# Performance work log

Measured on AMD Instinct MI355X. Metric: run time of the kernel, lower is better.

## Reference

```python
import jax, jax.numpy as jnp
import numpy as np

N = 50000
E = 800000
NODE_CONT = 64
EDGE_CAT = 16
HID = 96
LAT = 64
NUM_LAYERS = 2
BN_EPS = 1e-5


def setup_inputs() -> dict:
    key = jax.random.key(0)
    ks = jax.random.split(key, 24)
    s = 0.05
    inp = {
        "x_cont": jax.random.normal(ks[0], (N, NODE_CONT), jnp.float32),
        "x_cat": jax.random.randint(ks[1], (N,), 0, 1),
        "edge_index": jax.random.randint(ks[2], (2, E), 0, N),
        "edge_attr_cat": jax.random.randint(ks[3], (E,), 0, EDGE_CAT),
        "edge_attr_cont": jax.random.normal(ks[4], (E, 1), jnp.float32),
        # parameters
        "w_node": jax.random.normal(ks[5], (HID, NODE_CONT), jnp.float32) * s,
        "b_node": jnp.zeros((HID,), jnp.float32),
        "edge_embed": jax.random.normal(ks[6], (EDGE_CAT, HID), jnp.float32) * s,
        "gcn_w": jax.random.normal(ks[7], (NUM_LAYERS, HID, HID), jnp.float32) * s,
        "gcn_b": jnp.zeros((NUM_LAYERS, HID), jnp.float32),
        "bn_gamma": jnp.ones((NUM_LAYERS, HID), jnp.float32),
        "bn_beta": jnp.zeros((NUM_LAYERS, HID), jnp.float32),
        "mlp_w1": jax.random.normal(ks[8], (NUM_LAYERS, HID, 2 * HID), jnp.float32) * s,
        "mlp_b1": jnp.zeros((NUM_LAYERS, HID), jnp.float32),
        "mlp_w2": jax.random.normal(ks[9], (NUM_LAYERS, HID, HID), jnp.float32) * s,
        "mlp_b2": jnp.zeros((NUM_LAYERS, HID), jnp.float32),
        "mu_w": jax.random.normal(ks[10], (LAT, HID), jnp.float32) * s,
        "mu_b": jnp.zeros((LAT,), jnp.float32),
        "lv_w": jax.random.normal(ks[11], (LAT, HID), jnp.float32) * s,
        "lv_b": jnp.zeros((LAT,), jnp.float32),
    }
    return inp


def _forward(x_cont, edge_index, edge_attr_cat,
             w_node, b_node, edge_embed,
             gcn_w, gcn_b, bn_gamma, bn_beta,
             mlp_w1, mlp_b1, mlp_w2, mlp_b2,
             mu_w, mu_b, lv_w, lv_b):
    n = x_cont.shape[0]
    # node embed (only continuous path active)
    h = x_cont @ w_node.T + b_node                      # [N, H]
    # edge embed (only categorical path active) -- memory-bound gather
    edge_h = edge_embed[edge_attr_cat]                  # [E, H]
    src, dst = edge_index[0], edge_index[1]
    # GCNConv: add self-loops, symmetric normalization
    loop = jnp.arange(n)
    src_f = jnp.concatenate([src, loop])
    dst_f = jnp.concatenate([dst, loop])
    deg = jax.ops.segment_sum(jnp.ones_like(dst_f, jnp.float32), dst_f, num_segments=n)
    dinv = jax.lax.rsqrt(deg)                           # deg >= 1 (self loops)
    norm = (dinv[src_f] * dinv[dst_f])[:, None]         # [E+N, 1]
    # edge_pooled: O(E) segment-mean replacing the O(N*E) python loop;
    # edge_h is constant across layers so compute it once.
    cnt = jax.ops.segment_sum(jnp.ones((edge_h.shape[0],), edge_h.dtype), dst, num_segments=n)
    pooled = jax.ops.segment_sum(edge_h, dst, num_segments=n) / jnp.maximum(cnt, 1.0)[:, None]
    for l in range(gcn_w.shape[0]):
        msg = (h @ gcn_w[l].T)[src_f] * norm            # gather + scale
        h_gnn = jax.ops.segment_sum(msg, dst_f, num_segments=n) + gcn_b[l]
        hc = jnp.concatenate([h_gnn, pooled], axis=-1)  # [N, 2H]
        h = jax.nn.relu(hc @ mlp_w1[l].T + mlp_b1[l]) @ mlp_w2[l].T + mlp_b2[l]
        # BatchNorm1d (training-mode batch stats, biased variance)
        mean = jnp.mean(h, axis=0)
        var = jnp.mean((h - mean) ** 2, axis=0)
        h = (h - mean) * jax.lax.rsqrt(var + BN_EPS) * bn_gamma[l] + bn_beta[l]
        h = jax.nn.relu(h)
        # dropout: eval mode (identity)
    mu = h @ mu_w.T + mu_b
    logvar = h @ lv_w.T + lv_b
    return mu, logvar


def reference(x_cont, x_cat, edge_index, edge_attr_cat, edge_attr_cont,
              w_node, b_node, edge_embed, gcn_w, gcn_b, bn_gamma, bn_beta,
              mlp_w1, mlp_b1, mlp_w2, mlp_b2, mu_w, mu_b, lv_w, lv_b):
    # x_cat and edge_attr_cont are unused: in_node_cat_dim=0, in_edge_cont_dim=0
    return _forward(x_cont, edge_index, edge_attr_cat,
                    w_node, b_node, edge_embed,
                    gcn_w, gcn_b, bn_gamma, bn_beta,
                    mlp_w1, mlp_b1, mlp_w2, mlp_b2,
                    mu_w, mu_b, lv_w, lv_b)
```

## Files before the change

kernel.cpp:

```cpp
#include <hip/hip_runtime.h>

#define N_NODES 50000
#define N_EDGES 800000
#define HID 96
#define NODE_CONT 64
#define LATD 64
#define EDGE_CATN 16
#define BN_EPS 1e-5f
#define CPAD 16
#define BCAP 48
#define MLP_BLOCKS 625
#define PPITCH 640

typedef __attribute__((ext_vector_type(8))) short bf16x8;
typedef __attribute__((ext_vector_type(4))) float f32x4;

__device__ __forceinline__ unsigned short f2bf(float f) {
    union { float f; unsigned u; } c; c.f = f;
    unsigned r = (c.u + 0x7fffu + ((c.u >> 16) & 1u)) >> 16;
    return (unsigned short)r;
}
__device__ __forceinline__ float bf2f(unsigned short u) {
    union { unsigned u; float f; } c; c.u = ((unsigned)u) << 16;
    return c.f;
}

__global__ void k_build(const int* __restrict__ ei, const int* __restrict__ ecat,
                        int* __restrict__ cnt, int* __restrict__ csr) {
    int e = blockIdx.x * blockDim.x + threadIdx.x;
    if (e >= N_EDGES) return;
    int dst = ei[N_EDGES + e];
    int r = atomicAdd(&cnt[dst * CPAD], 1);
    if (r < BCAP) csr[(size_t)dst * BCAP + r] = (ei[e] << 4) | (ecat[e] & 15);
}

template<int POOL>
__global__ __launch_bounds__(256) void k_aggregate(
    const int* __restrict__ csr, const int* __restrict__ cnt,
    const unsigned short* __restrict__ bt,
    const float* __restrict__ gcn_b, unsigned short* __restrict__ bgp,
    const float* __restrict__ eemb)
{
    __shared__ float s_eemb[EDGE_CATN * HID];
    if constexpr (POOL) {
        for (int i = threadIdx.x; i < EDGE_CATN * HID; i += 256)
            s_eemb[i] = eemb[i];
        __syncthreads();
    }
    int node = blockIdx.x * 8 + (threadIdx.x >> 5);
    int lane = threadIdx.x & 31;
    if (node >= N_NODES) return;
    int degr = cnt[node * CPAD];
    float dd = rsqrtf((float)(degr + 1));
    int deg = degr > BCAP ? BCAP : degr;
    const unsigned short* tn = bt + (size_t)node * HID;
    float a0 = bf2f(tn[lane]);
    float a1 = bf2f(tn[lane + 32]);
    float a2 = bf2f(tn[lane + 64]);
    float p0 = 0.f, p1 = 0.f, p2 = 0.f;
    int beg = node * BCAP, end = beg + deg;
    int p = beg;
    for (; p + 4 <= end; p += 4) {
        int e0 = csr[p], e1 = csr[p + 1], e2 = csr[p + 2], e3 = csr[p + 3];
        const unsigned short* r0 = bt + (size_t)(e0 >> 4) * HID;
        const unsigned short* r1 = bt + (size_t)(e1 >> 4) * HID;
        const unsigned short* r2 = bt + (size_t)(e2 >> 4) * HID;
        const unsigned short* r3 = bt + (size_t)(e3 >> 4) * HID;
        unsigned short v00 = r0[lane], v01 = r0[lane + 32], v02 = r0[lane + 64];
        unsigned short v10 = r1[lane], v11 = r1[lane + 32], v12 = r1[lane + 64];
        unsigned short v20 = r2[lane], v21 = r2[lane + 32], v22 = r2[lane + 64];
        unsigned short v30 = r3[lane], v31 = r3[lane + 32], v32 = r3[lane + 64];
        a0 += (bf2f(v00) + bf2f(v10)) + (bf2f(v20) + bf2f(v30));
        a1 += (bf2f(v01) + bf2f(v11)) + (bf2f(v21) + bf2f(v31));
        a2 += (bf2f(v02) + bf2f(v12)) + (bf2f(v22) + bf2f(v32));
        if constexpr (POOL) {
            const float* q0 = s_eemb + (e0 & 15) * HID;
            const float* q1 = s_eemb + (e1 & 15) * HID;
            const float* q2 = s_eemb + (e2 & 15) * HID;
            const float* q3 = s_eemb + (e3 & 15) * HID;
            p0 += (q0[lane] + q1[lane]) + (q2[lane] + q3[lane]);
            p1 += (q0[lane + 32] + q1[lane + 32]) + (q2[lane + 32] + q3[lane + 32]);
            p2 += (q0[lane + 64] + q1[lane + 64]) + (q2[lane + 64] + q3[lane + 64]);
        }
    }
    for (; p < end; ++p) {
        int e0 = csr[p];
        const unsigned short* r = bt + (size_t)(e0 >> 4) * HID;
        a0 += bf2f(r[lane]);
        a1 += bf2f(r[lane + 32]);
        a2 += bf2f(r[lane + 64]);
        if constexpr (POOL) {
            const float* q = s_eemb + (e0 & 15) * HID;
            p0 += q[lane]; p1 += q[lane + 32]; p2 += q[lane + 64];
        }
    }
    unsigned short* o = bgp + (size_t)node * 192;
    o[lane]      = f2bf(a0 * dd + gcn_b[lane]);
    o[lane + 32] = f2bf(a1 * dd + gcn_b[lane + 32]);
    o[lane + 64] = f2bf(a2 * dd + gcn_b[lane + 64]);
    if constexpr (POOL) {
        float inv = 1.f / (float)(deg < 1 ? 1 : deg);
        unsigned short* ob = o + 96;
        ob[lane]      = f2bf(p0 * inv);
        ob[lane + 32] = f2bf(p1 * inv);
        ob[lane + 64] = f2bf(p2 * inv);
    }
}

#define OFF_WNODE 0
#define OFF_GCN   6144
#define OFF_W1    24576
#define OFF_W2    61440
#define OFF_MU    79872
#define W_TOTAL   92160

__device__ __forceinline__ void wf_decode(int e, int K, int njt, int& j, int& k) {
    int t = e & 7;
    int lane = (e >> 3) & 63;
    int g = e >> 9;
    int kb = g / njt;
    int jt = g - kb * njt;
    j = jt * 16 + (lane & 15);
    k = kb * 32 + (lane >> 4) * 8 + t;
}

__global__ void k_wprep(const float* __restrict__ w_node, const float* __restrict__ gcn_w,
                        const float* __restrict__ w1, const float* __restrict__ w2,
                        const float* __restrict__ mu_w, const float* __restrict__ lv_w,
                        const float* __restrict__ b_node,
                        unsigned short* __restrict__ out, float* __restrict__ fused_b) {
    int i = blockIdx.x * blockDim.x + threadIdx.x;
    if (i < OFF_GCN) {
        int j, k;
        wf_decode(i, NODE_CONT, 6, j, k);
        float s = 0.f;
#pragma unroll 8
        for (int q = 0; q < HID; ++q) s += gcn_w[j * HID + q] * w_node[q * NODE_CONT + k];
        out[i] = f2bf(s);
    } else if (i < OFF_W1) {
        int e = i - OFF_GCN;
        int l = e / 9216; e -= l * 9216;
        int j, k;
        wf_decode(e, HID, 6, j, k);
        out[i] = f2bf(gcn_w[l * HID * HID + j * HID + k]);
    } else if (i < OFF_W2) {
        int e = i - OFF_W1;
        int l = e / 18432; e -= l * 18432;
        int j, k;
        wf_decode(e, 192, 6, j, k);
        out[i] = f2bf(w1[l * HID * 192 + j * 192 + k]);
    } else if (i < OFF_MU) {
        int e = i - OFF_W2;
        int l = e / 9216; e -= l * 9216;
        int j, k;
        wf_decode(e, HID, 6, j, k);
        out[i] = f2bf(w2[l * HID * HID + j * HID + k]);
    } else if (i < W_TOTAL) {
        int e = i - OFF_MU;
        int j, k;
        wf_decode(e, HID, 8, j, k);
        float v = (j < 64) ? mu_w[j * HID + k] : lv_w[(j - 64) * HID + k];
        out[i] = f2bf(v);
    } else if (i < W_TOTAL + HID) {
        int j = i - W_TOTAL;
        float sb = 0.f;
#pragma unroll 8
        for (int q = 0; q < HID; ++q) sb += gcn_w[j * HID + q] * b_node[q];
        fused_b[j] = sb;
    }
}

template<int NJT, int AF32, int K1>
__global__ __launch_bounds__(320) void k_gemm_bf(
    const void* __restrict__ A1v,
    const float* __restrict__ ss,
    const unsigned short* __restrict__ Wb,
    const float* __restrict__ bias, const float* __restrict__ bias2,
    const int* __restrict__ cntp,
    unsigned short* __restrict__ Yb, float* __restrict__ Yf, float* __restrict__ Yf2,
    int act)
{
    constexpr int K = K1;
    const int tile = blockIdx.x * 5 + (threadIdx.x >> 6);
    const int lane = threadIdx.x & 63;
    const int m = lane & 15;
    const int kg = lane >> 4;

    f32x4 acc[NJT];
#pragma unroll
    for (int jt = 0; jt < NJT; ++jt) acc[jt] = (f32x4){0.f, 0.f, 0.f, 0.f};

    const int arow = tile * 16 + m;
    const unsigned short* wbase = Wb + lane * 8;

#pragma unroll
    for (int k0 = 0; k0 < K; k0 += 32) {
        int gk = k0 + kg * 8;
        bf16x8 a;
        if constexpr (AF32) {
            const float* apf = (const float*)A1v + (size_t)arow * K1 + gk;
            float4 x0 = *reinterpret_cast<const float4*>(apf);
            float4 x1 = *reinterpret_cast<const float4*>(apf + 4);
            a[0] = f2bf(x0.x); a[1] = f2bf(x0.y); a[2] = f2bf(x0.z); a[3] = f2bf(x0.w);
            a[4] = f2bf(x1.x); a[5] = f2bf(x1.y); a[6] = f2bf(x1.z); a[7] = f2bf(x1.w);
        } else {
            const unsigned short* ap = (const unsigned short*)A1v + (size_t)arow * K1 + gk;
            a = *reinterpret_cast<const bf16x8*>(ap);
            if (ss) {
#pragma unroll
                for (int i = 0; i < 8; ++i) {
                    float v = bf2f((unsigned short)a[i]);
                    v = fmaxf(v * ss[gk + i] + ss[96 + gk + i], 0.f);
                    a[i] = (short)f2bf(v);
                }
            }
        }
#pragma unroll
        for (int jt = 0; jt < NJT; ++jt) {
            bf16x8 b = *reinterpret_cast<const bf16x8*>(
                wbase + (((k0 >> 5) * NJT + jt) << 9));
            acc[jt] = __builtin_amdgcn_mfma_f32_16x16x32_bf16(a, b, acc[jt], 0, 0, 0);
        }
    }

    const int crow = tile * 16 + kg * 4;
    float rs[4] = {1.f, 1.f, 1.f, 1.f};
    if (cntp) {
#pragma unroll
        for (int r = 0; r < 4; ++r) rs[r] = rsqrtf((float)(cntp[(crow + r) * CPAD] + 1));
    }
#pragma unroll
    for (int jt = 0; jt < NJT; ++jt) {
        int j = jt * 16 + m;
        float bv = 0.f;
        if (Yf2) bv = (jt < NJT / 2) ? bias[j] : bias2[j - (NJT / 2) * 16];
        else if (bias) bv = bias[j];
#pragma unroll
        for (int r = 0; r < 4; ++r) {
            float v = acc[jt][r] + bv;
            if (act) v = fmaxf(v, 0.f);
            v *= rs[r];
            int row = crow + r;
            if (Yf2) {
                if (jt < NJT / 2) Yf[(size_t)row * ((NJT / 2) * 16) + j] = v;
                else              Yf2[(size_t)row * ((NJT / 2) * 16) + (j - (NJT / 2) * 16)] = v;
            } else {
                Yb[(size_t)row * (NJT * 16) + j] = f2bf(v);
            }
        }
    }
}

__global__ __launch_bounds__(320) void k_mlp(
    const unsigned short* __restrict__ A,
    const unsigned short* __restrict__ W1f, const float* __restrict__ b1,
    const unsigned short* __restrict__ W2f, const float* __restrict__ b2,
    unsigned short* __restrict__ bh, float* __restrict__ partials)
{
    __shared__ float s_stat[192];
    __shared__ unsigned short s_z1[5][16][104];
    for (int j = threadIdx.x; j < 192; j += 320) s_stat[j] = 0.f;
    const int wid = threadIdx.x >> 6;
    const int tile = blockIdx.x * 5 + wid;
    const int lane = threadIdx.x & 63;
    const int m = lane & 15;
    const int kg = lane >> 4;
    const int arow = tile * 16 + m;
    const unsigned short* w1base = W1f + lane * 8;
    const unsigned short* w2base = W2f + lane * 8;

    f32x4 acc[6];
#pragma unroll
    for (int jt = 0; jt < 6; ++jt) acc[jt] = (f32x4){0.f, 0.f, 0.f, 0.f};

    const unsigned short* ap = A + (size_t)arow * 192 + kg * 8;
#pragma unroll
    for (int k0 = 0; k0 < 192; k0 += 32) {
        bf16x8 a = *reinterpret_cast<const bf16x8*>(ap + k0);
#pragma unroll
        for (int jt = 0; jt < 6; ++jt) {
            bf16x8 b = *reinterpret_cast<const bf16x8*>(
                w1base + (((k0 >> 5) * 6 + jt) << 9));
            acc[jt] = __builtin_amdgcn_mfma_f32_16x16x32_bf16(a, b, acc[jt], 0, 0, 0);
        }
    }
#pragma unroll
    for (int jt = 0; jt < 6; ++jt) {
        int j = jt * 16 + m;
        float bv = b1[j];
#pragma unroll
        for (int r = 0; r < 4; ++r)
            s_z1[wid][kg * 4 + r][j] = f2bf(fmaxf(acc[jt][r] + bv, 0.f));
    }
    __syncthreads();

    f32x4 acc2[6];
#pragma unroll
    for (int jt = 0; jt < 6; ++jt) acc2[jt] = (f32x4){0.f, 0.f, 0.f, 0.f};
#pragma unroll
    for (int k0 = 0; k0 < 96; k0 += 32) {
        int gk = k0 + kg * 8;
        bf16x8 a = *reinterpret_cast<const bf16x8*>(&s_z1[wid][m][gk]);
#pragma unroll
        for (int jt = 0; jt < 6; ++jt) {
            bf16x8 b = *reinterpret_cast<const bf16x8*>(
                w2base + (((k0 >> 5) * 6 + jt) << 9));
            acc2[jt] = __builtin_amdgcn_mfma_f32_16x16x32_bf16(a, b, acc2[jt], 0, 0, 0);
        }
    }
    const int crow = tile * 16 + kg * 4;
#pragma unroll
    for (int jt = 0; jt < 6; ++jt) {
        int j = jt * 16 + m;
        float bv = b2[j];
        float lsum = 0.f, lsq = 0.f;
#pragma unroll
        for (int r = 0; r < 4; ++r) {
            float v = acc2[jt][r] + bv;
            lsum += v; lsq += v * v;
            bh[(size_t)(crow + r) * HID + j] = f2bf(v);
        }
        atomicAdd(&s_stat[j], lsum);
        atomicAdd(&s_stat[96 + j], lsq);
    }
    __syncthreads();
    for (int j = threadIdx.x; j < 192; j += 320)
        partials[(size_t)j * PPITCH + blockIdx.x] = s_stat[j];
}

__global__ __launch_bounds__(64) void k_bn_reduce(
    const float* __restrict__ partials,
    const float* __restrict__ g, const float* __restrict__ b,
    float* __restrict__ ss)
{
    int j = blockIdx.x;
    int t = threadIdx.x;
    float s = 0.f, s2 = 0.f;
    for (int i = t; i < MLP_BLOCKS; i += 64) {
        s  += partials[(size_t)j * PPITCH + i];
        s2 += partials[(size_t)(96 + j) * PPITCH + i];
    }
#pragma unroll
    for (int off = 32; off > 0; off >>= 1) {
        s  += __shfl_down(s, off, 64);
        s2 += __shfl_down(s2, off, 64);
    }
    if (t == 0) {
        float mean = s / (float)N_NODES;
        float var = s2 / (float)N_NODES - mean * mean;
        float sc = g[j] * rsqrtf(var + BN_EPS);
        ss[j] = sc;
        ss[96 + j] = b[j] - mean * sc;
    }
}

extern "C" void kernel_launch(void* const* d_in, const int* in_sizes, int n_in,
                              void* d_out, int out_size, void* d_ws, size_t ws_size,
                              hipStream_t stream) {
    const float* x_cont = (const float*)d_in[0];
    const int* edge_index = (const int*)d_in[2];
    const int* ecat = (const int*)d_in[3];
    const float* w_node = (const float*)d_in[5];
    const float* b_node = (const float*)d_in[6];
    const float* eemb = (const float*)d_in[7];
    const float* gcn_w = (const float*)d_in[8];
    const float* gcn_b = (const float*)d_in[9];
    const float* bn_g = (const float*)d_in[10];
    const float* bn_b = (const float*)d_in[11];
    const float* w1 = (const float*)d_in[12];
    const float* b1 = (const float*)d_in[13];
    const float* w2 = (const float*)d_in[14];
    const float* b2 = (const float*)d_in[15];
    const float* mu_w = (const float*)d_in[16];
    const float* mu_b = (const float*)d_in[17];
    const float* lv_w = (const float*)d_in[18];
    const float* lv_b = (const float*)d_in[19];
    float* out = (float*)d_out;

    char* base = (char*)d_ws;
    float* partials = (float*)base;                     base += (size_t)192 * PPITCH * 4;
    float* ssbuf    = (float*)base;                     base += 2 * 192 * 4;
    float* fused_b  = (float*)base;                     base += 128 * 4;
    int*   cnt      = (int*)base;                       base += (size_t)N_NODES * CPAD * 4;
    int*   csr      = (int*)base;                       base += (size_t)N_NODES * BCAP * 4;
    unsigned short* wbf = (unsigned short*)base;        base += (size_t)W_TOTAL * 2;
    unsigned short* bh  = (unsigned short*)base;        base += (size_t)N_NODES * HID * 2;
    unsigned short* bt  = (unsigned short*)base;        base += (size_t)N_NODES * HID * 2;
    unsigned short* bgp = (unsigned short*)base;        base += (size_t)N_NODES * 192 * 2;

    hipMemsetAsync(cnt, 0, (size_t)N_NODES * CPAD * sizeof(int), stream);

    k_wprep<<<(W_TOTAL + HID + 255) / 256, 256, 0, stream>>>(
        w_node, gcn_w, w1, w2, mu_w, lv_w, b_node, wbf, fused_b);
    k_build<<<(N_EDGES + 255) / 256, 256, 0, stream>>>(edge_index, ecat, cnt, csr);

    const int GG = N_NODES / 16 / 5;

    for (int l = 0; l < 2; ++l) {
        if (l == 0)
            k_gemm_bf<6, 1, NODE_CONT><<<GG, 320, 0, stream>>>(
                x_cont, nullptr, wbf + OFF_WNODE, fused_b, nullptr, cnt,
                bt, nullptr, nullptr, 0);
        else
            k_gemm_bf<6, 0, HID><<<GG, 320, 0, stream>>>(
                bh, ssbuf, wbf + OFF_GCN + l * HID * HID,
                nullptr, nullptr, cnt, bt, nullptr, nullptr, 0);
        if (l == 0)
            k_aggregate<1><<<N_NODES / 8, 256, 0, stream>>>(
                csr, cnt, bt, gcn_b + l * HID, bgp, eemb);
        else
            k_aggregate<0><<<N_NODES / 8, 256, 0, stream>>>(
                csr, cnt, bt, gcn_b + l * HID, bgp, eemb);
        k_mlp<<<GG, 320, 0, stream>>>(bgp,
                                      wbf + OFF_W1 + l * HID * 2 * HID, b1 + l * HID,
                                      wbf + OFF_W2 + l * HID * HID, b2 + l * HID,
                                      bh, partials);
        k_bn_reduce<<<96, 64, 0, stream>>>(partials, bn_g + l * HID, bn_b + l * HID,
                                           ssbuf + l * 192);
    }

    k_gemm_bf<8, 0, HID><<<GG, 320, 0, stream>>>(
        bh, ssbuf + 192, wbf + OFF_MU, mu_b, lv_b, nullptr,
        nullptr, out, out + (size_t)N_NODES * LATD, 0);
}
```

Baseline: 216.5 us.

## Split per-node edge buckets into four sub-counters to spread build atomics

New measurement: 252.4 us. 1.17x slower.

```diff
diff --git a/kernel.cpp b/kernel.cpp
--- a/kernel.cpp
+++ b/kernel.cpp
@@ -8,7 +8,8 @@
 #define EDGE_CATN 16
 #define BN_EPS 1e-5f
 #define CPAD 16
-#define BCAP 48
+#define SEGCAP 24
+#define BCAP4 96
 #define MLP_BLOCKS 625
 #define PPITCH 640
 
@@ -30,8 +31,10 @@
     int e = blockIdx.x * blockDim.x + threadIdx.x;
     if (e >= N_EDGES) return;
     int dst = ei[N_EDGES + e];
-    int r = atomicAdd(&cnt[dst * CPAD], 1);
-    if (r < BCAP) csr[(size_t)dst * BCAP + r] = (ei[e] << 4) | (ecat[e] & 15);
+    int s = e & 3;
+    int r = atomicAdd(&cnt[dst * CPAD + s], 1);
+    if (r < SEGCAP)
+        csr[(size_t)dst * BCAP4 + s * SEGCAP + r] = (ei[e] << 4) | (ecat[e] & 15);
 }
 
 template<int POOL>
@@ -50,48 +53,56 @@
     int node = blockIdx.x * 8 + (threadIdx.x >> 5);
     int lane = threadIdx.x & 31;
     if (node >= N_NODES) return;
-    int degr = cnt[node * CPAD];
-    float dd = rsqrtf((float)(degr + 1));
-    int deg = degr > BCAP ? BCAP : degr;
+    int4 c4 = *reinterpret_cast<const int4*>(cnt + (size_t)node * CPAD);
+    int tot = c4.x + c4.y + c4.z + c4.w;
+    float dd = rsqrtf((float)(tot + 1));
+    int c0 = c4.x < SEGCAP ? c4.x : SEGCAP;
+    int c1 = c4.y < SEGCAP ? c4.y : SEGCAP;
+    int c2 = c4.z < SEGCAP ? c4.z : SEGCAP;
+    int c3 = c4.w < SEGCAP ? c4.w : SEGCAP;
+    int cmax = max(max(c0, c1), max(c2, c3));
+    const int* bkt = csr + (size_t)node * BCAP4;
     const unsigned short* tn = bt + (size_t)node * HID;
     float a0 = bf2f(tn[lane]);
     float a1 = bf2f(tn[lane + 32]);
     float a2 = bf2f(tn[lane + 64]);
     float p0 = 0.f, p1 = 0.f, p2 = 0.f;
-    int beg = node * BCAP, end = beg + deg;
-    int p = beg;
-    for (; p + 4 <= end; p += 4) {
-        int e0 = csr[p], e1 = csr[p + 1], e2 = csr[p + 2], e3 = csr[p + 3];
-        const unsigned short* r0 = bt + (size_t)(e0 >> 4) * HID;
-        const unsigned short* r1 = bt + (size_t)(e1 >> 4) * HID;
-        const unsigned short* r2 = bt + (size_t)(e2 >> 4) * HID;
-        const unsigned short* r3 = bt + (size_t)(e3 >> 4) * HID;
-        unsigned short v00 = r0[lane], v01 = r0[lane + 32], v02 = r0[lane + 64];
-        unsigned short v10 = r1[lane], v11 = r1[lane + 32], v12 = r1[lane + 64];
-        unsigned short v20 = r2[lane], v21 = r2[lane + 32], v22 = r2[lane + 64];
-        unsigned short v30 = r3[lane], v31 = r3[lane + 32], v32 = r3[lane + 64];
-        a0 += (bf2f(v00) + bf2f(v10)) + (bf2f(v20) + bf2f(v30));
-        a1 += (bf2f(v01) + bf2f(v11)) + (bf2f(v21) + bf2f(v31));
-        a2 += (bf2f(v02) + bf2f(v12)) + (bf2f(v22) + bf2f(v32));
-        if constexpr (POOL) {
-            const float* q0 = s_eemb + (e0 & 15) * HID;
-            const float* q1 = s_eemb + (e1 & 15) * HID;
-            const float* q2 = s_eemb + (e2 & 15) * HID;
-            const float* q3 = s_eemb + (e3 & 15) * HID;
-            p0 += (q0[lane] + q1[lane]) + (q2[lane] + q3[lane]);
-            p1 += (q0[lane + 32] + q1[lane + 32]) + (q2[lane + 32] + q3[lane + 32]);
-            p2 += (q0[lane + 64] + q1[lane + 64]) + (q2[lane + 64] + q3[lane + 64]);
-        }
-    }
-    for (; p < end; ++p) {
-        int e0 = csr[p];
-        const unsigned short* r = bt + (size_t)(e0 >> 4) * HID;
-        a0 += bf2f(r[lane]);
-        a1 += bf2f(r[lane + 32]);
-        a2 += bf2f(r[lane + 64]);
-        if constexpr (POOL) {
-            const float* q = s_eemb + (e0 & 15) * HID;
-            p0 += q[lane]; p1 += q[lane + 32]; p2 += q[lane + 64];
+    for (int r = 0; r < cmax; ++r) {
+        int e0 = (r < c0) ? bkt[r] : -1;
+        int e1 = (r < c1) ? bkt[SEGCAP + r] : -1;
+        int e2 = (r < c2) ? bkt[2 * SEGCAP + r] : -1;
+        int e3 = (r < c3) ? bkt[3 * SEGCAP + r] : -1;
+        if (e0 >= 0) {
+            const unsigned short* rr = bt + (size_t)(e0 >> 4) * HID;
+            a0 += bf2f(rr[lane]); a1 += bf2f(rr[lane + 32]); a2 += bf2f(rr[lane + 64]);
+            if constexpr (POOL) {
+                const float* q = s_eemb + (e0 & 15) * HID;
+                p0 += q[lane]; p1 += q[lane + 32]; p2 += q[lane + 64];
+            }
+        }
+        if (e1 >= 0) {
+            const unsigned short* rr = bt + (size_t)(e1 >> 4) * HID;
+            a0 += bf2f(rr[lane]); a1 += bf2f(rr[lane + 32]); a2 += bf2f(rr[lane + 64]);
+            if constexpr (POOL) {
+                const float* q = s_eemb + (e1 & 15) * HID;
+                p0 += q[lane]; p1 += q[lane + 32]; p2 += q[lane + 64];
+            }
+        }
+        if (e2 >= 0) {
+            const unsigned short* rr = bt + (size_t)(e2 >> 4) * HID;
+            a0 += bf2f(rr[lane]); a1 += bf2f(rr[lane + 32]); a2 += bf2f(rr[lane + 64]);
+            if constexpr (POOL) {
+                const float* q = s_eemb + (e2 & 15) * HID;
+                p0 += q[lane]; p1 += q[lane + 32]; p2 += q[lane + 64];
+            }
+        }
+        if (e3 >= 0) {
+            const unsigned short* rr = bt + (size_t)(e3 >> 4) * HID;
+            a0 += bf2f(rr[lane]); a1 += bf2f(rr[lane + 32]); a2 += bf2f(rr[lane + 64]);
+            if constexpr (POOL) {
+                const float* q = s_eemb + (e3 & 15) * HID;
+                p0 += q[lane]; p1 += q[lane + 32]; p2 += q[lane + 64];
+            }
         }
     }
     unsigned short* o = bgp + (size_t)node * 192;
@@ -99,7 +110,7 @@
     o[lane + 32] = f2bf(a1 * dd + gcn_b[lane + 32]);
     o[lane + 64] = f2bf(a2 * dd + gcn_b[lane + 64]);
     if constexpr (POOL) {
-        float inv = 1.f / (float)(deg < 1 ? 1 : deg);
+        float inv = 1.f / (float)(tot < 1 ? 1 : tot);
         unsigned short* ob = o + 96;
         ob[lane]      = f2bf(p0 * inv);
         ob[lane + 32] = f2bf(p1 * inv);
@@ -227,7 +238,10 @@
     float rs[4] = {1.f, 1.f, 1.f, 1.f};
     if (cntp) {
 #pragma unroll
-        for (int r = 0; r < 4; ++r) rs[r] = rsqrtf((float)(cntp[(crow + r) * CPAD] + 1));
+        for (int r = 0; r < 4; ++r) {
+            int4 c4 = *reinterpret_cast<const int4*>(cntp + (size_t)(crow + r) * CPAD);
+            rs[r] = rsqrtf((float)(c4.x + c4.y + c4.z + c4.w + 1));
+        }
     }
 #pragma unroll
     for (int jt = 0; jt < NJT; ++jt) {
@@ -382,7 +396,7 @@
     float* ssbuf    = (float*)base;                     base += 2 * 192 * 4;
     float* fused_b  = (float*)base;                     base += 128 * 4;
     int*   cnt      = (int*)base;                       base += (size_t)N_NODES * CPAD * 4;
-    int*   csr      = (int*)base;                       base += (size_t)N_NODES * BCAP * 4;
+    int*   csr      = (int*)base;                       base += (size_t)N_NODES * BCAP4 * 4;
     unsigned short* wbf = (unsigned short*)base;        base += (size_t)W_TOTAL * 2;
     unsigned short* bh  = (unsigned short*)base;        base += (size_t)N_NODES * HID * 2;
     unsigned short* bt  = (unsigned short*)base;        base += (size_t)N_NODES * HID * 2;
```

## Split edge-bucket atomics into eight sub-counters and compact into CSR

Applied to the files above, without the earlier changes.

New measurement: 224.3 us. 1.04x slower.

```diff
diff --git a/kernel.cpp b/kernel.cpp
--- a/kernel.cpp
+++ b/kernel.cpp
@@ -8,6 +8,9 @@
 #define EDGE_CATN 16
 #define BN_EPS 1e-5f
 #define CPAD 16
+#define NSEG 8
+#define SEGCAP 16
+#define SEGTOT 128
 #define BCAP 48
 #define MLP_BLOCKS 625
 #define PPITCH 640
@@ -26,17 +29,52 @@
 }
 
 __global__ void k_build(const int* __restrict__ ei, const int* __restrict__ ecat,
-                        int* __restrict__ cnt, int* __restrict__ csr) {
+                        int* __restrict__ cnt, int* __restrict__ csrS) {
     int e = blockIdx.x * blockDim.x + threadIdx.x;
     if (e >= N_EDGES) return;
     int dst = ei[N_EDGES + e];
-    int r = atomicAdd(&cnt[dst * CPAD], 1);
-    if (r < BCAP) csr[(size_t)dst * BCAP + r] = (ei[e] << 4) | (ecat[e] & 15);
+    int s = e & (NSEG - 1);
+    int r = atomicAdd(&cnt[dst * CPAD + s], 1);
+    if (r < SEGCAP)
+        csrS[(size_t)dst * SEGTOT + s * SEGCAP + r] = (ei[e] << 4) | (ecat[e] & 15);
+}
+
+__global__ __launch_bounds__(256) void k_compact(
+    const int* __restrict__ cnt, const int* __restrict__ csrS,
+    int* __restrict__ csr, int* __restrict__ deg, float* __restrict__ dinv)
+{
+    int node = blockIdx.x * 8 + (threadIdx.x >> 5);
+    int lane = threadIdx.x & 31;
+    if (node >= N_NODES) return;
+    int c[NSEG];
+    int degT = 0;
+    int base[NSEG + 1];
+    base[0] = 0;
+#pragma unroll
+    for (int s = 0; s < NSEG; ++s) {
+        c[s] = cnt[(size_t)node * CPAD + s];
+        degT += c[s];
+        int cc = c[s] < SEGCAP ? c[s] : SEGCAP;
+        base[s + 1] = base[s] + cc;
+    }
+    int total = base[NSEG] < BCAP ? base[NSEG] : BCAP;
+    for (int r = lane; r < total; r += 32) {
+        int s = 0;
+#pragma unroll
+        for (int q = 0; q < NSEG - 1; ++q) s += (r >= base[q + 1]) ? 1 : 0;
+        csr[(size_t)node * BCAP + r] =
+            csrS[(size_t)node * SEGTOT + s * SEGCAP + (r - base[s])];
+    }
+    if (lane == 0) {
+        deg[node] = total;
+        dinv[node] = rsqrtf((float)(degT + 1));
+    }
 }
 
 template<int POOL>
 __global__ __launch_bounds__(256) void k_aggregate(
-    const int* __restrict__ csr, const int* __restrict__ cnt,
+    const int* __restrict__ csr, const int* __restrict__ deg,
+    const float* __restrict__ dinv,
     const unsigned short* __restrict__ bt,
     const float* __restrict__ gcn_b, unsigned short* __restrict__ bgp,
     const float* __restrict__ eemb)
@@ -50,15 +88,14 @@
     int node = blockIdx.x * 8 + (threadIdx.x >> 5);
     int lane = threadIdx.x & 31;
     if (node >= N_NODES) return;
-    int degr = cnt[node * CPAD];
-    float dd = rsqrtf((float)(degr + 1));
-    int deg = degr > BCAP ? BCAP : degr;
+    float dd = dinv[node];
+    int dg = deg[node];
     const unsigned short* tn = bt + (size_t)node * HID;
     float a0 = bf2f(tn[lane]);
     float a1 = bf2f(tn[lane + 32]);
     float a2 = bf2f(tn[lane + 64]);
     float p0 = 0.f, p1 = 0.f, p2 = 0.f;
-    int beg = node * BCAP, end = beg + deg;
+    int beg = node * BCAP, end = beg + dg;
     int p = beg;
     for (; p + 4 <= end; p += 4) {
         int e0 = csr[p], e1 = csr[p + 1], e2 = csr[p + 2], e3 = csr[p + 3];
@@ -99,7 +136,7 @@
     o[lane + 32] = f2bf(a1 * dd + gcn_b[lane + 32]);
     o[lane + 64] = f2bf(a2 * dd + gcn_b[lane + 64]);
     if constexpr (POOL) {
-        float inv = 1.f / (float)(deg < 1 ? 1 : deg);
+        float inv = 1.f / (float)(dg < 1 ? 1 : dg);
         unsigned short* ob = o + 96;
         ob[lane]      = f2bf(p0 * inv);
         ob[lane + 32] = f2bf(p1 * inv);
@@ -176,7 +213,7 @@
     const float* __restrict__ ss,
     const unsigned short* __restrict__ Wb,
     const float* __restrict__ bias, const float* __restrict__ bias2,
-    const int* __restrict__ cntp,
+    const float* __restrict__ rowscale,
     unsigned short* __restrict__ Yb, float* __restrict__ Yf, float* __restrict__ Yf2,
     int act)
 {
@@ -225,9 +262,9 @@
 
     const int crow = tile * 16 + kg * 4;
     float rs[4] = {1.f, 1.f, 1.f, 1.f};
-    if (cntp) {
-#pragma unroll
-        for (int r = 0; r < 4; ++r) rs[r] = rsqrtf((float)(cntp[(crow + r) * CPAD] + 1));
+    if (rowscale) {
+#pragma unroll
+        for (int r = 0; r < 4; ++r) rs[r] = rowscale[crow + r];
     }
 #pragma unroll
     for (int jt = 0; jt < NJT; ++jt) {
@@ -381,7 +418,10 @@
     float* partials = (float*)base;                     base += (size_t)192 * PPITCH * 4;
     float* ssbuf    = (float*)base;                     base += 2 * 192 * 4;
     float* fused_b  = (float*)base;                     base += 128 * 4;
+    float* dinv     = (float*)base;                     base += (size_t)N_NODES * 4;
+    int*   deg      = (int*)base;                       base += (size_t)N_NODES * 4;
     int*   cnt      = (int*)base;                       base += (size_t)N_NODES * CPAD * 4;
+    int*   csrS     = (int*)base;                       base += (size_t)N_NODES * SEGTOT * 4;
     int*   csr      = (int*)base;                       base += (size_t)N_NODES * BCAP * 4;
     unsigned short* wbf = (unsigned short*)base;        base += (size_t)W_TOTAL * 2;
     unsigned short* bh  = (unsigned short*)base;        base += (size_t)N_NODES * HID * 2;
@@ -392,25 +432,26 @@
 
     k_wprep<<<(W_TOTAL + HID + 255) / 256, 256, 0, stream>>>(
         w_node, gcn_w, w1, w2, mu_w, lv_w, b_node, wbf, fused_b);
-    k_build<<<(N_EDGES + 255) / 256, 256, 0, stream>>>(edge_index, ecat, cnt, csr);
+    k_build<<<(N_EDGES + 255) / 256, 256, 0, stream>>>(edge_index, ecat, cnt, csrS);
+    k_compact<<<(N_NODES + 7) / 8, 256, 0, stream>>>(cnt, csrS, csr, deg, dinv);
 
     const int GG = N_NODES / 16 / 5;
 
     for (int l = 0; l < 2; ++l) {
         if (l == 0)
             k_gemm_bf<6, 1, NODE_CONT><<<GG, 320, 0, stream>>>(
-                x_cont, nullptr, wbf + OFF_WNODE, fused_b, nullptr, cnt,
+                x_cont, nullptr, wbf + OFF_WNODE, fused_b, nullptr, dinv,
                 bt, nullptr, nullptr, 0);
         else
             k_gemm_bf<6, 0, HID><<<GG, 320, 0, stream>>>(
                 bh, ssbuf, wbf + OFF_GCN + l * HID * HID,
-                nullptr, nullptr, cnt, bt, nullptr, nullptr, 0);
+                nullptr, nullptr, dinv, bt, nullptr, nullptr, 0);
         if (l == 0)
             k_aggregate<1><<<N_NODES / 8, 256, 0, stream>>>(
-                csr, cnt, bt, gcn_b + l * HID, bgp, eemb);
+                csr, deg, dinv, bt, gcn_b + l * HID, bgp, eemb);
         else
             k_aggregate<0><<<N_NODES / 8, 256, 0, stream>>>(
-                csr, cnt, bt, gcn_b + l * HID, bgp, eemb);
+                csr, deg, dinv, bt, gcn_b + l * HID, bgp, eemb);
         k_mlp<<<GG, 320, 0, stream>>>(bgp,
                                       wbf + OFF_W1 + l * HID * 2 * HID, b1 + l * HID,
                                       wbf + OFF_W2 + l * HID * HID, b2 + l * HID,
```
